# Optimization experiments

Measured on AMD Instinct MI355X. Metric: run time of the kernel, lower is better.

Reference implementation:

```python
import jax, jax.numpy as jnp
import numpy as np
from jax import lax

DIM = 256
NI, NS, NP = 8, 4, 16
H = W = 36
SCALE = 20.0
POOL = 4
EPS_BN = 1e-5


def setup_inputs() -> dict:
    key = jax.random.key(0)
    ks = jax.random.split(key, 20)
    feat = jax.random.normal(ks[0], (NI, NS, DIM, H, W), jnp.float32)
    # proposals in xywh; scaled by 20 inside PrRoIPool, so keep boxes inside the 36x36 map
    xy = jax.random.uniform(ks[1], (NI, NS, NP, 2), jnp.float32) * 1.2
    wh = 0.1 + jax.random.uniform(ks[2], (NI, NS, NP, 2), jnp.float32) * 0.4
    proposals = jnp.concatenate([xy, wh], axis=-1)

    def kaiming(k, shape, fan_in):
        return jax.random.normal(k, shape, jnp.float32) * np.float32(np.sqrt(2.0 / fan_in))

    d = dict(feat=feat, proposals=proposals)
    for i, name in enumerate(['conv1', 'conv2', 'conv3']):
        d[name + '_w'] = kaiming(ks[3 + i], (DIM, DIM, 3, 3), DIM * 9)
        d[name + '_b'] = jnp.zeros((DIM,), jnp.float32)
        d['bn%d_g' % (i + 1)] = jax.random.uniform(ks[6 + i], (DIM,), jnp.float32)
        d['bn%d_b' % (i + 1)] = jnp.zeros((DIM,), jnp.float32)
    d['fc_w'] = kaiming(ks[9], (DIM, DIM * POOL * POOL), DIM * POOL * POOL)
    d['fc_b'] = jnp.zeros((DIM,), jnp.float32)
    d['fcbn_g'] = jax.random.uniform(ks[10], (DIM,), jnp.float32)
    d['fcbn_b'] = jnp.zeros((DIM,), jnp.float32)
    d['iou_w'] = kaiming(ks[11], (1, DIM), DIM)
    d['iou_b'] = jnp.zeros((1,), jnp.float32)
    return d


def _cbr(x, w, b, g, beta):
    # Conv(3x3, pad 1) + BatchNorm (training-mode batch stats) + ReLU
    x = lax.conv_general_dilated(x, w, (1, 1), ((1, 1), (1, 1)),
                                 dimension_numbers=('NCHW', 'OIHW', 'NCHW'))
    x = x + b[None, :, None, None]
    m = x.mean((0, 2, 3), keepdims=True)
    v = x.var((0, 2, 3), keepdims=True)
    x = (x - m) / jnp.sqrt(v + EPS_BN) * g[None, :, None, None] + beta[None, :, None, None]
    return jax.nn.relu(x)


def _trapcum_last(a):
    # trapezoidal cumulative integral along last axis, value 0 at index 0
    mid = 0.5 * (a[..., :-1] + a[..., 1:])
    return jnp.concatenate([jnp.zeros_like(a[..., :1]), jnp.cumsum(mid, axis=-1)], axis=-1)


def _prroi_pool(feat, rois, pooled=POOL, scale=SCALE):
    # Precise RoI pooling: exact double integral of the bilinear interpolant per bin,
    # computed analytically via trapezoidal cumulative integrals of the feature map.
    N, C, Hh, Ww = feat.shape
    Ux = _trapcum_last(feat)                                            # int_0^x f
    Uy = jnp.swapaxes(_trapcum_last(jnp.swapaxes(feat, -1, -2)), -1, -2)  # int_0^y f
    T = jnp.swapaxes(_trapcum_last(jnp.swapaxes(Ux, -1, -2)), -1, -2)     # int_0^y int_0^x f

    b = rois[:, 0].astype(jnp.int32)
    x1, y1, x2, y2 = (rois[:, 1] * scale, rois[:, 2] * scale,
                      rois[:, 3] * scale, rois[:, 4] * scale)
    bw = (x2 - x1) / pooled
    bh = (y2 - y1) / pooled
    grid = jnp.arange(pooled + 1, dtype=feat.dtype)
    xs = jnp.clip(x1[:, None] + bw[:, None] * grid, 0.0, Ww - 1)        # (R, P+1)
    ys = jnp.clip(y1[:, None] + bh[:, None] * grid, 0.0, Hh - 1)
    wx = jnp.clip(jnp.floor(xs), 0, Ww - 2).astype(jnp.int32)
    hy = jnp.clip(jnp.floor(ys), 0, Hh - 2).astype(jnp.int32)
    sx = xs - wx.astype(feat.dtype)
    sy = ys - hy.astype(feat.dtype)
    px1 = 0.5 * sx * sx
    px0 = sx - px1
    py1 = 0.5 * sy * sy
    py0 = sy - py1

    def g(arr, hi, wi):
        # gather per-RoI values -> (R, P+1, P+1, C), rows index y, cols index x
        return arr[b[:, None, None], :, hi[:, :, None], wi[:, None, :]]

    px0e = px0[:, None, :, None]
    px1e = px1[:, None, :, None]
    py0e = py0[:, :, None, None]
    py1e = py1[:, :, None, None]
    h0, h1 = hy, hy + 1
    w0, w1 = wx, wx + 1
    # antiderivative G(X, Y) = int_0^Y int_0^X f of the bilinear interpolant
    G = (g(T, h0, w0)
         + g(Uy, h0, w0) * px0e + g(Uy, h0, w1) * px1e
         + py0e * (g(Ux, h0, w0) + g(feat, h0, w0) * px0e + g(feat, h0, w1) * px1e)
         + py1e * (g(Ux, h1, w0) + g(feat, h1, w0) * px0e + g(feat, h1, w1) * px1e))
    # per-bin integral via inclusion-exclusion on the (P+1)x(P+1) corner grid
    d = G[:, 1:, 1:] - G[:, :-1, 1:] - G[:, 1:, :-1] + G[:, :-1, :-1]   # (R, P, P, C)
    area = (bw * bh)[:, None, None, None]
    out = jnp.where(area > 1e-8, d / jnp.maximum(area, 1e-8), 0.0)
    return jnp.transpose(out, (0, 3, 1, 2))  # (R, C, P, P)


def reference(feat, proposals, conv1_w, conv1_b, bn1_g, bn1_b, conv2_w, conv2_b,
              bn2_g, bn2_b, conv3_w, conv3_b, bn3_g, bn3_b, fc_w, fc_b,
              fcbn_g, fcbn_b, iou_w, iou_b):
    ni, ns = proposals.shape[0], proposals.shape[1]
    x = feat.reshape(-1, *feat.shape[-3:])
    x = _cbr(x, conv1_w, conv1_b, bn1_g, bn1_b)
    x = _cbr(x, conv2_w, conv2_b, bn2_g, bn2_b)
    x = _cbr(x, conv3_w, conv3_b, bn3_g, bn3_b)

    props = proposals.reshape(ni * ns, -1, 4)
    B, P = props.shape[0], props.shape[1]
    xyxy = jnp.concatenate([props[..., 0:2], props[..., 0:2] + props[..., 2:4]], axis=-1)
    bidx = jnp.broadcast_to(jnp.arange(B, dtype=props.dtype)[:, None, None], (B, P, 1))
    rois = jnp.concatenate([bidx, xyxy], axis=-1).reshape(-1, 5)

    rf = _prroi_pool(x, rois)                       # (B*P, C, 4, 4)
    fcx = rf.reshape(rf.shape[0], -1) @ fc_w.T + fc_b
    m = fcx.mean(0)
    v = fcx.var(0)
    fcx = jax.nn.relu((fcx - m) / jnp.sqrt(v + EPS_BN) * fcbn_g + fcbn_b)
    iou = fcx @ iou_w.T + iou_b                     # (B*P, 1)
    return iou.reshape(ni, ns, -1)
```

## Files before the change

kernel.cpp:

```cpp
#include <hip/hip_runtime.h>
#include <hip/hip_bf16.h>
#include <stdint.h>

#define CDIM 256
#define HH 36
#define WW 36
#define NPX 1296
#define PW 38
#define PPIX 1444
#define NIMG 32
#define NROI 512
#define FCK 4096
#define EPS_BN 1e-5f
#define SBLK 192

typedef __bf16 bf16;
typedef __bf16 bf16x8 __attribute__((ext_vector_type(8)));
typedef float f32x4 __attribute__((ext_vector_type(4)));
typedef unsigned short us8 __attribute__((ext_vector_type(8)));

#define GLD16(g, l) __builtin_amdgcn_global_load_lds( \
    (__attribute__((address_space(1))) void*)(g),     \
    (__attribute__((address_space(3))) void*)(l), 16, 0, 0)

__global__ void k_wconv3(const float* __restrict__ w0, const float* __restrict__ w1,
                         const float* __restrict__ w2, bf16* __restrict__ wb) {
  int l = blockIdx.y;
  const float* ws = (l == 0) ? w0 : (l == 1) ? w1 : w2;
  bf16* dst = wb + (size_t)l * 9 * CDIM * CDIM;
  int i = blockIdx.x * 256 + threadIdx.x;
  if (i >= 9 * CDIM * CDIM) return;
  int tap = i / (CDIM * CDIM);
  int rem = i - tap * (CDIM * CDIM);
  int co = rem >> 8, ci = rem & 255;
  dst[i] = (bf16)ws[(size_t)(co * CDIM + ci) * 9 + tap];
}

__global__ void k_cast(const float* __restrict__ src, bf16* __restrict__ dst, int nElem) {
  int i = blockIdx.x * 256 + threadIdx.x;
  if (i < nElem) dst[i] = (bf16)src[i];
}

__global__ void k_convert(const float* __restrict__ feat, bf16* __restrict__ xp) {
  __shared__ bf16 tile[CDIM * 38];
  int h = blockIdx.x, n = blockIdx.y, t = threadIdx.x;
  const float* src = feat + (size_t)n * CDIM * NPX + (size_t)h * WW;
#pragma unroll 4
  for (int i = 0; i < 36; ++i) {
    int f = i * 256 + t;
    int c = (int)(((unsigned)f * 7282u) >> 18);
    int w = f - c * 36;
    tile[c * 38 + w] = (bf16)src[(size_t)c * NPX + w];
  }
  __syncthreads();
  bf16* dst = xp + (size_t)n * PPIX * CDIM + ((h + 1) * PW + 1) * CDIM + t;
#pragma unroll 4
  for (int w = 0; w < 36; ++w) dst[w * CDIM] = tile[t * 38 + w];
}

__global__ __launch_bounds__(256) void k_conv(
    const bf16* __restrict__ xp, const bf16* __restrict__ wb,
    bf16* __restrict__ y)
{
  __shared__ __align__(16) bf16 ldsA[2][4096];
  __shared__ __align__(16) bf16 ldsB[2][4096];
  const int tid = threadIdx.x;
  const int wave = tid >> 6, lane = tid & 63;
  const int pxt = blockIdx.x, cot = blockIdx.y, n = blockIdx.z;

  const int q = lane >> 2;
  const int gsw = (lane & 3) ^ ((q >> 1) & 3);
  const int rA = wave * 32 + q;
  const bf16* aS0 = wb + (size_t)(cot * 128 + rA) * CDIM + gsw * 8;
  const bf16* aS1 = aS0 + 16 * CDIM;
  int pxa = pxt * 128 + rA;       if (pxa > NPX - 1) pxa = NPX - 1;
  int pxb = pxt * 128 + rA + 16;  if (pxb > NPX - 1) pxb = NPX - 1;
  const int ha = pxa / 36, wa = pxa - ha * 36;
  const int hb = pxb / 36, wbv = pxb - hb * 36;
  const bf16* bS0 = xp + (size_t)n * (PPIX * CDIM) + ((ha + 1) * PW + (wa + 1)) * CDIM + gsw * 8;
  const bf16* bS1 = xp + (size_t)n * (PPIX * CDIM) + ((hb + 1) * PW + (wbv + 1)) * CDIM + gsw * 8;

  const int fr = lane & 15, fg = lane >> 4;
  const int fsw = (fg ^ ((fr >> 1) & 3)) * 8;
  const int wco = wave >> 1, wpx = wave & 1;
  const int aoff = (wco * 64 + fr) * 32 + fsw;
  const int boff = (wpx * 64 + fr) * 32 + fsw;

  f32x4 acc[4][4];
#pragma unroll
  for (int i = 0; i < 4; ++i)
#pragma unroll
    for (int j = 0; j < 4; ++j) acc[i][j] = f32x4{0.f, 0.f, 0.f, 0.f};

  {
    const int xoff = -(PW + 1) * CDIM;
    GLD16(aS0, &ldsA[0][wave * 1024]);
    GLD16(aS1, &ldsA[0][wave * 1024 + 512]);
    GLD16(bS0 + xoff, &ldsB[0][wave * 1024]);
    GLD16(bS1 + xoff, &ldsB[0][wave * 1024 + 512]);
  }

#pragma unroll 2
  for (int k = 0; k < 72; ++k) {
    const int buf = k & 1;
    __syncthreads();
    if (k + 1 < 72) {
      const int kn = k + 1;
      const int tap = kn >> 3, ci0 = (kn & 7) << 5;
      const int dh = tap / 3 - 1, dw = tap - (tap / 3) * 3 - 1;
      const int woff = tap * (CDIM * CDIM) + ci0;
      const int xoff = (dh * PW + dw) * CDIM + ci0;
      const int nb = buf ^ 1;
      GLD16(aS0 + woff, &ldsA[nb][wave * 1024]);
      GLD16(aS1 + woff, &ldsA[nb][wave * 1024 + 512]);
      GLD16(bS0 + xoff, &ldsB[nb][wave * 1024]);
      GLD16(bS1 + xoff, &ldsB[nb][wave * 1024 + 512]);
    }
    bf16x8 av[4], bv[4];
#pragma unroll
    for (int i = 0; i < 4; ++i) av[i] = *(const bf16x8*)&ldsA[buf][aoff + i * 512];
#pragma unroll
    for (int j = 0; j < 4; ++j) bv[j] = *(const bf16x8*)&ldsB[buf][boff + j * 512];
#pragma unroll
    for (int i = 0; i < 4; ++i)
#pragma unroll
      for (int j = 0; j < 4; ++j)
        acc[i][j] = __builtin_amdgcn_mfma_f32_16x16x32_bf16(av[i], bv[j], acc[i][j], 0, 0, 0);
  }

#pragma unroll
  for (int j = 0; j < 4; ++j) {
    const int px = pxt * 128 + wpx * 64 + j * 16 + fr;
    if (px < NPX) {
      bf16* dst = y + ((size_t)n * NPX + px) * CDIM + cot * 128 + wco * 64 + fg * 4;
#pragma unroll
      for (int i = 0; i < 4; ++i) {
        f32x4 a = acc[i][j];
        union { bf16 b4[4]; ushort4 u4; } pk;
        pk.b4[0] = (bf16)a[0]; pk.b4[1] = (bf16)a[1];
        pk.b4[2] = (bf16)a[2]; pk.b4[3] = (bf16)a[3];
        *(ushort4*)(dst + i * 16) = pk.u4;
      }
    }
  }
}

__global__ void k_statsb(const bf16* __restrict__ y, float* __restrict__ psum,
                         float* __restrict__ psq) {
  __shared__ float lsum[8][256];
  __shared__ float lsq[8][256];
  int t = threadIdx.x;
  int c8 = (t & 31) * 8, rg = t >> 5;
  size_t row0 = (size_t)blockIdx.x * 216 + rg;
  float s[8], qq[8];
#pragma unroll
  for (int k = 0; k < 8; ++k) { s[k] = 0.f; qq[k] = 0.f; }
  for (int i = 0; i < 27; ++i) {
    const bf16* p = y + (row0 + (size_t)i * 8) * CDIM + c8;
    union { bf16 b8[8]; us8 u; } v;
    v.u = *(const us8*)p;
#pragma unroll
    for (int k = 0; k < 8; ++k) {
      float f = (float)v.b8[k];
      s[k] += f; qq[k] += f * f;
    }
  }
#pragma unroll
  for (int k = 0; k < 8; ++k) { lsum[rg][c8 + k] = s[k]; lsq[rg][c8 + k] = qq[k]; }
  __syncthreads();
  float ss = 0.f, sq2 = 0.f;
#pragma unroll
  for (int g = 0; g < 8; ++g) { ss += lsum[g][t]; sq2 += lsq[g][t]; }
  psum[blockIdx.x * 256 + t] = ss;
  psq[blockIdx.x * 256 + t] = sq2;
}

__global__ void k_sred(const float* __restrict__ psum, const float* __restrict__ psq,
                       float* __restrict__ su, float* __restrict__ sq) {
  int c = threadIdx.x;
  float s = 0.f, q = 0.f;
  for (int i = 0; i < SBLK; ++i) { s += psum[i * 256 + c]; q += psq[i * 256 + c]; }
  su[c] = s; sq[c] = q;
}

__global__ void k_stats(const float* __restrict__ x, float* __restrict__ sum,
                        float* __restrict__ ssq, int rpb) {
  int c = threadIdx.x;
  size_t base = (size_t)blockIdx.x * rpb;
  float s = 0.f, s2 = 0.f;
  for (int i = 0; i < rpb; ++i) {
    float v = x[(base + i) * CDIM + c];
    s += v; s2 += v * v;
  }
  atomicAdd(&sum[c], s);
  atomicAdd(&ssq[c], s2);
}

__global__ void k_finalize(const float* __restrict__ sum, const float* __restrict__ ssq,
                           const float* __restrict__ g, const float* __restrict__ b,
                           float* __restrict__ sc, float* __restrict__ sh, float invn) {
  int c = threadIdx.x;
  float m = sum[c] * invn;
  float v = ssq[c] * invn - m * m;
  float s = g[c] * rsqrtf(v + EPS_BN);
  sc[c] = s;
  sh[c] = b[c] - m * s;
}

__global__ void k_normalize(const bf16* __restrict__ y, const float* __restrict__ sc,
                            const float* __restrict__ sh, bf16* __restrict__ xp) {
  int t = threadIdx.x;
  int n = blockIdx.y;
  int px = blockIdx.x * 8 + (t >> 5);
  int c8 = (t & 31) * 8;
  const bf16* srcp = y + ((size_t)n * NPX + px) * CDIM + c8;
  union { bf16 b8[8]; us8 u; } in, outp;
  in.u = *(const us8*)srcp;
  int h = px / 36, w = px - h * 36;
#pragma unroll
  for (int i = 0; i < 8; ++i) {
    float v = (float)in.b8[i];
    outp.b8[i] = (bf16)fmaxf(v * sc[c8 + i] + sh[c8 + i], 0.f);
  }
  *(us8*)(xp + (size_t)n * PPIX * CDIM + ((h + 1) * PW + (w + 1)) * CDIM + c8) = outp.u;
}

__device__ __forceinline__ float hatH(float u) {
  u = fminf(fmaxf(u, -1.f), 1.f);
  float p = u + 1.f;
  return (u < 0.f) ? 0.5f * p * p : 0.5f + u * (1.f - 0.5f * u);
}

__global__ __launch_bounds__(128) void k_pool(
    const bf16* __restrict__ y, const float* __restrict__ sc,
    const float* __restrict__ sh, const float* __restrict__ props,
    bf16* __restrict__ rf) {
  int roi = blockIdx.x;
  int c = blockIdx.y * 128 + threadIdx.x;
  int b = roi >> 4;
  const float* pr = props + (size_t)roi * 4;
  float x1 = pr[0] * 20.f, yy1 = pr[1] * 20.f;
  float x2 = (pr[0] + pr[2]) * 20.f, yy2 = (pr[1] + pr[3]) * 20.f;
  float bw = (x2 - x1) * 0.25f, bh = (yy2 - yy1) * 0.25f;

  float xs[5], ys[5];
#pragma unroll
  for (int j = 0; j < 5; ++j) {
    xs[j] = fminf(fmaxf(x1 + bw * j, 0.f), 35.f);
    ys[j] = fminf(fmaxf(yy1 + bh * j, 0.f), 35.f);
  }
  float wxv[4][5], wyv[4][5];
  int sx[4], sy[4];
#pragma unroll
  for (int j = 0; j < 4; ++j) {
    float a = xs[j], bb = xs[j + 1];
    int s = (int)floorf(a);
    sx[j] = s;
#pragma unroll
    for (int k = 0; k < 5; ++k) {
      float w = (float)(s + k);
      wxv[j][k] = hatH(bb - w) - hatH(a - w);
    }
    float ay = ys[j], by = ys[j + 1];
    int t = (int)floorf(ay);
    sy[j] = t;
#pragma unroll
    for (int k = 0; k < 5; ++k) {
      float w = (float)(t + k);
      wyv[j][k] = hatH(by - w) - hatH(ay - w);
    }
  }

  float s_ = sc[c], t_ = sh[c];
  const bf16* yb = y + (size_t)b * NPX * CDIM + c;
  float acc[4][4];
#pragma unroll
  for (int i = 0; i < 4; ++i)
#pragma unroll
    for (int j = 0; j < 4; ++j) acc[i][j] = 0.f;

#pragma unroll
  for (int i = 0; i < 4; ++i) {
#pragma unroll
    for (int ky = 0; ky < 5; ++ky) {
      float wy = wyv[i][ky];
      if (wy == 0.f) continue;
      int h = sy[i] + ky; if (h > 35) h = 35;
      const bf16* rowp = yb + h * (WW * CDIM);
#pragma unroll
      for (int j = 0; j < 4; ++j) {
        float rd = 0.f;
#pragma unroll
        for (int kx = 0; kx < 5; ++kx) {
          int w = sx[j] + kx; if (w > 35) w = 35;
          float f = fmaxf((float)rowp[w * CDIM] * s_ + t_, 0.f);
          rd += wxv[j][kx] * f;
        }
        acc[i][j] += wy * rd;
      }
    }
  }

  float area = bw * bh;
  float inv = area > 1e-8f ? 1.f / area : 0.f;
  bf16 outv[16];
#pragma unroll
  for (int i = 0; i < 4; ++i)
#pragma unroll
    for (int j = 0; j < 4; ++j)
      outv[i * 4 + j] = (bf16)(acc[i][j] * inv);
  bf16* dst = rf + (size_t)roi * FCK + c * 16;
  *(us8*)(dst)     = *(us8*)&outv[0];
  *(us8*)(dst + 8) = *(us8*)&outv[8];
}

__global__ __launch_bounds__(256) void k_fcgemm(const bf16* __restrict__ rf,
                                                const bf16* __restrict__ fw,
                                                float* __restrict__ fcp) {
  int tid = threadIdx.x, wave = tid >> 6, lane = tid & 63;
  int wo = wave >> 1, wr = wave & 1;
  int rt = blockIdx.x, ot = blockIdx.y, ks = blockIdx.z;
  int fr = lane & 15, fg = lane >> 4;
  const bf16* ap = fw + (size_t)(ot * 64 + wo * 32 + fr) * FCK + ks * 512 + fg * 8;
  const bf16* bp = rf + (size_t)(rt * 64 + wr * 32 + fr) * FCK + ks * 512 + fg * 8;
  f32x4 acc[2][2];
#pragma unroll
  for (int i = 0; i < 2; ++i)
#pragma unroll
    for (int j = 0; j < 2; ++j) acc[i][j] = f32x4{0.f, 0.f, 0.f, 0.f};
#pragma unroll 4
  for (int k = 0; k < 512; k += 32) {
    bf16x8 a0 = *(const bf16x8*)(ap + k);
    bf16x8 a1 = *(const bf16x8*)(ap + 16 * FCK + k);
    bf16x8 b0 = *(const bf16x8*)(bp + k);
    bf16x8 b1 = *(const bf16x8*)(bp + 16 * FCK + k);
    acc[0][0] = __builtin_amdgcn_mfma_f32_16x16x32_bf16(a0, b0, acc[0][0], 0, 0, 0);
    acc[0][1] = __builtin_amdgcn_mfma_f32_16x16x32_bf16(a0, b1, acc[0][1], 0, 0, 0);
    acc[1][0] = __builtin_amdgcn_mfma_f32_16x16x32_bf16(a1, b0, acc[1][0], 0, 0, 0);
    acc[1][1] = __builtin_amdgcn_mfma_f32_16x16x32_bf16(a1, b1, acc[1][1], 0, 0, 0);
  }
#pragma unroll
  for (int i = 0; i < 2; ++i)
#pragma unroll
    for (int j = 0; j < 2; ++j) {
      int o = ot * 64 + wo * 32 + i * 16 + fg * 4;
      int r = rt * 64 + wr * 32 + j * 16 + fr;
      *(f32x4*)(fcp + ((size_t)ks * NROI + r) * CDIM + o) = acc[i][j];
    }
}

__global__ void k_fcred(const float* __restrict__ fcp, float* __restrict__ fcx) {
  int r = blockIdx.x, o = threadIdx.x;
  float s = 0.f;
#pragma unroll
  for (int ks = 0; ks < 8; ++ks) s += fcp[((size_t)ks * NROI + r) * CDIM + o];
  fcx[(size_t)r * CDIM + o] = s;
}

__global__ void k_iou(const float* __restrict__ fcx, const float* __restrict__ sc,
                      const float* __restrict__ sh, const float* __restrict__ iw,
                      const float* __restrict__ ib, float* __restrict__ out) {
  __shared__ float red[4];
  int roi = blockIdx.x, t = threadIdx.x;
  float v = fcx[(size_t)roi * CDIM + t];
  v = fmaxf(v * sc[t] + sh[t], 0.f) * iw[t];
#pragma unroll
  for (int o = 32; o > 0; o >>= 1) v += __shfl_down(v, o);
  if ((t & 63) == 0) red[t >> 6] = v;
  __syncthreads();
  if (t == 0) out[roi] = red[0] + red[1] + red[2] + red[3] + ib[0];
}

extern "C" void kernel_launch(void* const* d_in, const int* in_sizes, int n_in,
                              void* d_out, int out_size, void* d_ws, size_t ws_size,
                              hipStream_t stream) {
  (void)in_sizes; (void)n_in; (void)out_size;
  const float* feat  = (const float*)d_in[0];
  const float* props = (const float*)d_in[1];
  const float* convw[3] = {(const float*)d_in[2], (const float*)d_in[6], (const float*)d_in[10]};
  const float* bng[3]   = {(const float*)d_in[4], (const float*)d_in[8], (const float*)d_in[12]};
  const float* bnb[3]   = {(const float*)d_in[5], (const float*)d_in[9], (const float*)d_in[13]};
  const float* fcw  = (const float*)d_in[14];
  const float* fcg  = (const float*)d_in[16];
  const float* fcbb = (const float*)d_in[17];
  const float* iw   = (const float*)d_in[18];
  const float* ib   = (const float*)d_in[19];
  float* out = (float*)d_out;

  char* w = (char*)d_ws;
  size_t off = 0;
  auto take = [&](size_t sz) -> char* { char* p = w + off; off += (sz + 255) & ~(size_t)255; return p; };
  const size_t SZ_XP = (size_t)NIMG * PPIX * CDIM * 2;
  const size_t SZ_YB = (size_t)NIMG * NPX * CDIM * 2;
  const size_t SZ_P  = (size_t)SBLK * 256 * 4;
  bf16*  xp0 = (bf16*)take(SZ_XP);
  bf16*  xp1 = (bf16*)take(SZ_XP);
  bf16*  y   = (bf16*)take(SZ_YB);
  bf16*  wball = (bf16*)take((size_t)3 * 9 * CDIM * CDIM * 2);
  bf16*  fwb = (bf16*)take((size_t)CDIM * FCK * 2);
  bf16*  rfb = (bf16*)take((size_t)NROI * FCK * 2);
  float* fcx = (float*)take((size_t)NROI * CDIM * 4);
  float* fcp = (float*)take((size_t)8 * NROI * CDIM * 4);
  float* psum = (float*)take(SZ_P);
  float* psq  = (float*)take(SZ_P);
  float* stat = (float*)take(8 * 256 * 4);
  float* scsh = (float*)take(8 * 256 * 4);
  if (off > ws_size) return;

  hipMemsetAsync(xp0, 0, SZ_XP * 2, stream);
  hipMemsetAsync(stat, 0, 8 * 256 * 4, stream);

  k_wconv3<<<dim3(2304, 3), 256, 0, stream>>>(convw[0], convw[1], convw[2], wball);
  k_cast<<<dim3(4096), 256, 0, stream>>>(fcw, fwb, CDIM * FCK);
  k_convert<<<dim3(HH, NIMG), 256, 0, stream>>>(feat, xp0);

  for (int l = 0; l < 3; ++l) {
    bf16* xin = (l == 1) ? xp1 : xp0;
    bf16* wbl = wball + (size_t)l * 9 * CDIM * CDIM;
    k_conv<<<dim3(11, 2, NIMG), 256, 0, stream>>>(xin, wbl, y);
    float* su = stat + l * 512; float* sq = su + 256;
    k_statsb<<<dim3(SBLK), 256, 0, stream>>>(y, psum, psq);
    k_sred<<<dim3(1), 256, 0, stream>>>(psum, psq, su, sq);
    float* sc = scsh + l * 512; float* sh = sc + 256;
    k_finalize<<<dim3(1), 256, 0, stream>>>(su, sq, bng[l], bnb[l], sc, sh, 1.f / 41472.f);
    if (l < 2) {
      bf16* xo = (l == 0) ? xp1 : xp0;
      k_normalize<<<dim3(NPX / 8, NIMG), 256, 0, stream>>>(y, sc, sh, xo);
    }
  }
  float* sc3 = scsh + 2 * 512; float* sh3 = sc3 + 256;
  k_pool<<<dim3(NROI, 2), 128, 0, stream>>>(y, sc3, sh3, props, rfb);
  k_fcgemm<<<dim3(8, 4, 8), 256, 0, stream>>>(rfb, fwb, fcp);
  k_fcred<<<dim3(NROI), 256, 0, stream>>>(fcp, fcx);
  float* fsu = stat + 3 * 512; float* fsq = fsu + 256;
  k_stats<<<dim3(8), 256, 0, stream>>>(fcx, fsu, fsq, 64);
  float* fsc = scsh + 3 * 512; float* fsh = fsc + 256;
  k_finalize<<<dim3(1), 256, 0, stream>>>(fsu, fsq, fcg, fcbb, fsc, fsh, 1.f / 512.f);
  k_iou<<<dim3(NROI), 256, 0, stream>>>(fcx, fsc, fsh, iw, ib, out);
}
```

Before: 490.2 us.

## Fuse small prep/stat kernels and remap conv blocks for XCD-aware scheduling

Merges the conv-weight and FC-weight casting kernels into one launch, fuses the BN partial reduction with finalization, replaces the atomic-based FC stats with a single-block reduce+finalize, and drops a memset. It also flattens the conv grid to 1D and remaps block IDs so each XCD handles whole images, which should improve L2 locality for weights and activations. The changes reduce launch count and host overhead, at the cost of a serial single-block FC stats loop.

```diff
diff --git a/kernel.cpp b/kernel.cpp
--- a/kernel.cpp
+++ b/kernel.cpp
@@ -13,6 +13,7 @@
 #define FCK 4096
 #define EPS_BN 1e-5f
 #define SBLK 192
+#define NWC (9*CDIM*CDIM)
 
 typedef __bf16 bf16;
 typedef __bf16 bf16x8 __attribute__((ext_vector_type(8)));
@@ -23,22 +24,21 @@
     (__attribute__((address_space(1))) void*)(g),     \
     (__attribute__((address_space(3))) void*)(l), 16, 0, 0)
 
-__global__ void k_wconv3(const float* __restrict__ w0, const float* __restrict__ w1,
-                         const float* __restrict__ w2, bf16* __restrict__ wb) {
-  int l = blockIdx.y;
-  const float* ws = (l == 0) ? w0 : (l == 1) ? w1 : w2;
-  bf16* dst = wb + (size_t)l * 9 * CDIM * CDIM;
+__global__ void k_prep(const float* __restrict__ w0, const float* __restrict__ w1,
+                       const float* __restrict__ w2, const float* __restrict__ fcw,
+                       bf16* __restrict__ wb, bf16* __restrict__ fwb) {
   int i = blockIdx.x * 256 + threadIdx.x;
-  if (i >= 9 * CDIM * CDIM) return;
-  int tap = i / (CDIM * CDIM);
-  int rem = i - tap * (CDIM * CDIM);
-  int co = rem >> 8, ci = rem & 255;
-  dst[i] = (bf16)ws[(size_t)(co * CDIM + ci) * 9 + tap];
-}
-
-__global__ void k_cast(const float* __restrict__ src, bf16* __restrict__ dst, int nElem) {
-  int i = blockIdx.x * 256 + threadIdx.x;
-  if (i < nElem) dst[i] = (bf16)src[i];
+  if (i < 3 * NWC) {
+    int l = i / NWC, r = i - l * NWC;
+    const float* ws = (l == 0) ? w0 : (l == 1) ? w1 : w2;
+    int tap = r / (CDIM * CDIM);
+    int rem = r - tap * (CDIM * CDIM);
+    int co = rem >> 8, ci = rem & 255;
+    wb[i] = (bf16)ws[(size_t)(co * CDIM + ci) * 9 + tap];
+  } else {
+    int j = i - 3 * NWC;
+    if (j < CDIM * FCK) fwb[j] = (bf16)fcw[j];
+  }
 }
 
 __global__ void k_convert(const float* __restrict__ feat, bf16* __restrict__ xp) {
@@ -66,7 +66,12 @@
   __shared__ __align__(16) bf16 ldsB[2][4096];
   const int tid = threadIdx.x;
   const int wave = tid >> 6, lane = tid & 63;
-  const int pxt = blockIdx.x, cot = blockIdx.y, n = blockIdx.z;
+
+  const int B = blockIdx.x;
+  const int xcd = B & 7, idx = B >> 3;
+  const int ng = idx / 22, inner = idx - ng * 22;
+  const int n = (ng << 3) + xcd;
+  const int cot = inner / 11, pxt = inner - cot * 11;
 
   const int q = lane >> 2;
   const int gsw = (lane & 3) ^ ((q >> 1) & 3);
@@ -175,36 +180,17 @@
   psq[blockIdx.x * 256 + t] = sq2;
 }
 
-__global__ void k_sred(const float* __restrict__ psum, const float* __restrict__ psq,
-                       float* __restrict__ su, float* __restrict__ sq) {
+__global__ void k_sredfin(const float* __restrict__ psum, const float* __restrict__ psq,
+                          const float* __restrict__ g, const float* __restrict__ b,
+                          float* __restrict__ sc, float* __restrict__ sh, float invn) {
   int c = threadIdx.x;
   float s = 0.f, q = 0.f;
   for (int i = 0; i < SBLK; ++i) { s += psum[i * 256 + c]; q += psq[i * 256 + c]; }
-  su[c] = s; sq[c] = q;
-}
-
-__global__ void k_stats(const float* __restrict__ x, float* __restrict__ sum,
-                        float* __restrict__ ssq, int rpb) {
-  int c = threadIdx.x;
-  size_t base = (size_t)blockIdx.x * rpb;
-  float s = 0.f, s2 = 0.f;
-  for (int i = 0; i < rpb; ++i) {
-    float v = x[(base + i) * CDIM + c];
-    s += v; s2 += v * v;
-  }
-  atomicAdd(&sum[c], s);
-  atomicAdd(&ssq[c], s2);
-}
-
-__global__ void k_finalize(const float* __restrict__ sum, const float* __restrict__ ssq,
-                           const float* __restrict__ g, const float* __restrict__ b,
-                           float* __restrict__ sc, float* __restrict__ sh, float invn) {
-  int c = threadIdx.x;
-  float m = sum[c] * invn;
-  float v = ssq[c] * invn - m * m;
-  float s = g[c] * rsqrtf(v + EPS_BN);
-  sc[c] = s;
-  sh[c] = b[c] - m * s;
+  float m = s * invn;
+  float v = q * invn - m * m;
+  float sca = g[c] * rsqrtf(v + EPS_BN);
+  sc[c] = sca;
+  sh[c] = b[c] - m * sca;
 }
 
 __global__ void k_normalize(const bf16* __restrict__ y, const float* __restrict__ sc,
@@ -355,6 +341,22 @@
 #pragma unroll
   for (int ks = 0; ks < 8; ++ks) s += fcp[((size_t)ks * NROI + r) * CDIM + o];
   fcx[(size_t)r * CDIM + o] = s;
+}
+
+__global__ void k_fcstatfin(const float* __restrict__ fcx, const float* __restrict__ g,
+                            const float* __restrict__ b, float* __restrict__ sc,
+                            float* __restrict__ sh) {
+  int c = threadIdx.x;
+  float s = 0.f, q = 0.f;
+  for (int r = 0; r < NROI; ++r) {
+    float v = fcx[(size_t)r * CDIM + c];
+    s += v; q += v * v;
+  }
+  float m = s * (1.f / 512.f);
+  float vv = q * (1.f / 512.f) - m * m;
+  float sca = g[c] * rsqrtf(vv + EPS_BN);
+  sc[c] = sca;
+  sh[c] = b[c] - m * sca;
 }
 
 __global__ void k_iou(const float* __restrict__ fcx, const float* __restrict__ sc,
@@ -396,33 +398,29 @@
   bf16*  xp0 = (bf16*)take(SZ_XP);
   bf16*  xp1 = (bf16*)take(SZ_XP);
   bf16*  y   = (bf16*)take(SZ_YB);
-  bf16*  wball = (bf16*)take((size_t)3 * 9 * CDIM * CDIM * 2);
+  bf16*  wball = (bf16*)take((size_t)3 * NWC * 2);
   bf16*  fwb = (bf16*)take((size_t)CDIM * FCK * 2);
   bf16*  rfb = (bf16*)take((size_t)NROI * FCK * 2);
   float* fcx = (float*)take((size_t)NROI * CDIM * 4);
   float* fcp = (float*)take((size_t)8 * NROI * CDIM * 4);
   float* psum = (float*)take(SZ_P);
   float* psq  = (float*)take(SZ_P);
-  float* stat = (float*)take(8 * 256 * 4);
   float* scsh = (float*)take(8 * 256 * 4);
   if (off > ws_size) return;
 
   hipMemsetAsync(xp0, 0, SZ_XP * 2, stream);
-  hipMemsetAsync(stat, 0, 8 * 256 * 4, stream);
-
-  k_wconv3<<<dim3(2304, 3), 256, 0, stream>>>(convw[0], convw[1], convw[2], wball);
-  k_cast<<<dim3(4096), 256, 0, stream>>>(fcw, fwb, CDIM * FCK);
+
+  k_prep<<<dim3((3 * NWC + CDIM * FCK + 255) / 256), 256, 0, stream>>>(
+      convw[0], convw[1], convw[2], fcw, wball, fwb);
   k_convert<<<dim3(HH, NIMG), 256, 0, stream>>>(feat, xp0);
 
   for (int l = 0; l < 3; ++l) {
     bf16* xin = (l == 1) ? xp1 : xp0;
-    bf16* wbl = wball + (size_t)l * 9 * CDIM * CDIM;
-    k_conv<<<dim3(11, 2, NIMG), 256, 0, stream>>>(xin, wbl, y);
-    float* su = stat + l * 512; float* sq = su + 256;
+    bf16* wbl = wball + (size_t)l * NWC;
+    k_conv<<<dim3(704), 256, 0, stream>>>(xin, wbl, y);
     k_statsb<<<dim3(SBLK), 256, 0, stream>>>(y, psum, psq);
-    k_sred<<<dim3(1), 256, 0, stream>>>(psum, psq, su, sq);
     float* sc = scsh + l * 512; float* sh = sc + 256;
-    k_finalize<<<dim3(1), 256, 0, stream>>>(su, sq, bng[l], bnb[l], sc, sh, 1.f / 41472.f);
+    k_sredfin<<<dim3(1), 256, 0, stream>>>(psum, psq, bng[l], bnb[l], sc, sh, 1.f / 41472.f);
     if (l < 2) {
       bf16* xo = (l == 0) ? xp1 : xp0;
       k_normalize<<<dim3(NPX / 8, NIMG), 256, 0, stream>>>(y, sc, sh, xo);
@@ -432,9 +430,7 @@
   k_pool<<<dim3(NROI, 2), 128, 0, stream>>>(y, sc3, sh3, props, rfb);
   k_fcgemm<<<dim3(8, 4, 8), 256, 0, stream>>>(rfb, fwb, fcp);
   k_fcred<<<dim3(NROI), 256, 0, stream>>>(fcp, fcx);
-  float* fsu = stat + 3 * 512; float* fsq = fsu + 256;
-  k_stats<<<dim3(8), 256, 0, stream>>>(fcx, fsu, fsq, 64);
   float* fsc = scsh + 3 * 512; float* fsh = fsc + 256;
-  k_finalize<<<dim3(1), 256, 0, stream>>>(fsu, fsq, fcg, fcbb, fsc, fsh, 1.f / 512.f);
+  k_fcstatfin<<<dim3(1), 256, 0, stream>>>(fcx, fcg, fcbb, fsc, fsh);
   k_iou<<<dim3(NROI), 256, 0, stream>>>(fcx, fsc, fsh, iw, ib, out);
 }
```

After: 462.0 us. -5.8%, faster.
